# Kernel optimization log

Measured on AMD Instinct MI355X. Metric: run time of the kernel, lower is better.

Reference implementation:

```python
import jax, jax.numpy as jnp
import numpy as np

B_SZ = 8
D_MODEL = 512
D_STATE = 64
N2 = D_STATE // 2  # S4D uses complex-conjugate pairs -> d_state//2 complex modes
L_SEQ = 2048


def setup_inputs() -> dict:
    key = jax.random.key(0)
    ks = jax.random.split(key, 16)
    d = D_MODEL
    scale = 1.0 / np.sqrt(d)
    inp = {
        "x": jax.random.normal(ks[0], (B_SZ, d, L_SEQ), dtype=jnp.float32),
        # q/k/v projections (nn.Linear: weight (out,in), bias (out,))
        "Wq": jax.random.normal(ks[1], (d, d), dtype=jnp.float32) * scale,
        "bq": jax.random.normal(ks[2], (d,), dtype=jnp.float32) * scale,
        "Wk": jax.random.normal(ks[3], (d, d), dtype=jnp.float32) * scale,
        "bk": jax.random.normal(ks[4], (d,), dtype=jnp.float32) * scale,
        "Wv": jax.random.normal(ks[5], (d, d), dtype=jnp.float32) * scale,
        "bv": jax.random.normal(ks[6], (d,), dtype=jnp.float32) * scale,
        # Shift layer params
        "shift_C": jax.random.normal(ks[7], (1, d, D_STATE), dtype=jnp.float32),
        "shift_D": jax.random.normal(ks[8], (d,), dtype=jnp.float32),
        # S4D (diagonal SSM) params
        "log_dt": jax.random.uniform(ks[9], (d,), dtype=jnp.float32,
                                      minval=np.log(1e-3), maxval=np.log(1e-1)),
        "A_real": jnp.log(0.5 * jnp.ones((d, N2), dtype=jnp.float32)),
        "A_imag": jnp.broadcast_to(np.pi * jnp.arange(N2, dtype=jnp.float32), (d, N2)),
        "C_re": jax.random.normal(ks[10], (d, N2), dtype=jnp.float32) * np.sqrt(0.5),
        "C_im": jax.random.normal(ks[11], (d, N2), dtype=jnp.float32) * np.sqrt(0.5),
        "s4_D": jax.random.normal(ks[12], (d,), dtype=jnp.float32),
    }
    return inp


def _linear_chan(x, W, b):
    # x: (B, H, L); Linear applied over channel dim H -> (B, H_out, L)
    return jnp.einsum("bhl,dh->bdl", x, W) + b[:, None]


def _shift(u, C, Dp):
    """Shift SSM: causal conv with kernel = first L taps of C (computed via FFT
    exactly as the torch source does). u: (B, H, L)."""
    L = u.shape[-1]
    n = 2 * L
    H, S = C.shape[1], C.shape[2]
    Bmat = jnp.zeros((H, S), dtype=u.dtype).at[:, 0].set(1.0)
    B_fc = jnp.conj(jnp.fft.rfft(Bmat, n=n, axis=-1))  # (H, L+1)
    C_f = jnp.fft.rfft(C, n=n, axis=-1)                # (1, H, L+1)
    kernel = jnp.fft.irfft(B_fc * C_f, n=n, axis=-1)[..., :L]  # (1, H, L)
    kernel_f = jnp.fft.rfft(kernel, n=n, axis=-1)      # (1, H, L+1)
    u_f = jnp.fft.rfft(u, n=n, axis=-1)                # (B, H, L+1)
    y = jnp.fft.irfft(u_f * kernel_f, n=n, axis=-1)[..., :L]
    return y + u * Dp[:, None]


def _s4d(u, log_dt, A_real, A_imag, C_re, C_im, Dp):
    """Standard S4D forward: ZOH-discretized diagonal SSM kernel + FFT conv.
    u: (B, H, L)."""
    L = u.shape[-1]
    n = 2 * L
    dt = jnp.exp(log_dt)[:, None]                  # (H, 1)
    A = -jnp.exp(A_real) + 1j * A_imag             # (H, N2)
    dtA = A * dt                                   # (H, N2)
    C = (C_re + 1j * C_im) * (jnp.exp(dtA) - 1.0) / A
    vand = jnp.exp(dtA[:, :, None] * jnp.arange(L))  # (H, N2, L)
    K = 2.0 * jnp.einsum("hn,hnl->hl", C, vand).real  # (H, L)
    y = jnp.fft.irfft(jnp.fft.rfft(u, n=n, axis=-1) * jnp.fft.rfft(K, n=n, axis=-1),
                      n=n, axis=-1)[..., :L]
    return y + u * Dp[:, None]


def reference(x, Wq, bq, Wk, bk, Wv, bv, shift_C, shift_D,
              log_dt, A_real, A_imag, C_re, C_im, s4_D):
    q = _linear_chan(x, Wq, bq)
    k = _linear_chan(x, Wk, bk)
    v = _linear_chan(x, Wv, bv)
    shift_out = _shift(k, shift_C, shift_D)
    s4d_out = _s4d(v * shift_out, log_dt, A_real, A_imag, C_re, C_im, s4_D)
    return q * s4d_out
```

## Files before the change

kernel.cpp:

```cpp
#include <hip/hip_runtime.h>
#include <cstdint>


#define DMODEL 512
#define LSEQ 2048

typedef _Float16 half_t;
typedef __attribute__((ext_vector_type(4))) _Float16 half4v;
typedef __attribute__((ext_vector_type(8))) _Float16 half8v;
typedef __attribute__((ext_vector_type(4))) float floatx4;

#define SW(R, c) ((R) * 64 + ((((c) >> 3) ^ ((R) & 7)) << 3) + ((c) & 7))

__device__ __forceinline__ void gload_lds16(const half_t* g, half_t* l) {
  __builtin_amdgcn_global_load_lds(
      (const __attribute__((address_space(1))) uint32_t*)g,
      (__attribute__((address_space(3))) uint32_t*)l, 16, 0, 0);
}

__global__ __launch_bounds__(256) void convert_w(
    const float* __restrict__ Wq, const float* __restrict__ Wk,
    const float* __restrict__ Wv, half_t* __restrict__ W16) {
  int i = blockIdx.x * 256 + threadIdx.x;
  const float* src = (i < 262144) ? Wq : ((i < 524288) ? Wk : Wv);
  int j = i & 262143;
  W16[i] = (half_t)src[j];
}

__global__ __launch_bounds__(256) void transpose_x(
    const float* __restrict__ x, half_t* __restrict__ xT) {
  __shared__ float tile[64][68];
  int b = blockIdx.z;
  int d0 = blockIdx.y * 64;
  int l0 = blockIdx.x * 64;
  int t = threadIdx.x;
  int dy = t >> 4, lx = t & 15;
  const float* xp = x + ((size_t)(b * 512 + d0)) * 2048 + l0;
#pragma unroll
  for (int rr = 0; rr < 4; rr++) {
    float4 v = *(const float4*)(xp + (size_t)(rr * 16 + dy) * 2048 + lx * 4);
    *(float4*)&tile[rr * 16 + dy][lx * 4] = v;
  }
  __syncthreads();
  half_t* op = xT + ((size_t)(b * 2048 + l0)) * 512 + d0;
  int lr = t >> 2, c4 = t & 3;
#pragma unroll
  for (int cc = 0; cc < 2; cc++) {
    int ch = cc * 4 + c4;
    half8v hv;
#pragma unroll
    for (int e = 0; e < 8; e++) hv[e] = (half_t)tile[ch * 8 + e][lr];
    *(half8v*)(op + (size_t)lr * 512 + ch * 8) = hv;
  }
}

__global__ __launch_bounds__(256) void s4d_tables(
    const float* __restrict__ log_dt, const float* __restrict__ A_real,
    const float* __restrict__ A_imag, const float* __restrict__ C_re,
    const float* __restrict__ C_im, const float* __restrict__ shC,
    half_t* __restrict__ Vt, half_t* __restrict__ Et, half_t* __restrict__ Tt,
    half_t* __restrict__ T1t, half_t* __restrict__ T2t,
    float* __restrict__ wt2) {
  __shared__ float aL[32], bL[32], wrL[32], wiL[32], crL[32], ciL[32];
  __shared__ float Kt[64], tapl[64];
  int h = blockIdx.x;
  int tid = threadIdx.x;
  if (tid < 64) { Kt[tid] = 0.f; tapl[tid] = shC[h * 64 + tid]; }
  if (tid < 32) {
    int n = tid, hn = h * 32 + n;
    float dt = expf(log_dt[h]);
    float Ar = -expf(A_real[hn]), Ai = A_imag[hn];
    float a = dt * Ar, b = dt * Ai;
    float ea = expf(a);
    float wr = ea * cosf(b), wi = ea * sinf(b);
    float Am2 = Ar * Ar + Ai * Ai;
    float zr = wr - 1.0f, zi = wi;
    float qr = (zr * Ar + zi * Ai) / Am2;
    float qi = (zi * Ar - zr * Ai) / Am2;
    aL[n] = a; bL[n] = b; wrL[n] = wr; wiL[n] = wi;
    crL[n] = C_re[hn] * qr - C_im[hn] * qi;
    ciL[n] = C_re[hn] * qi + C_im[hn] * qr;
    float e64 = expf(64.0f * a);
    wt2[h * 64 + 2 * n]     = e64 * cosf(64.0f * b);
    wt2[h * 64 + 2 * n + 1] = e64 * sinf(64.0f * b);
  }
  __syncthreads();
  size_t base = (size_t)h * 4096;
  {
    int r = tid >> 2;
    int nb = (tid & 3) * 8;
    float ksum = 0.f;
#pragma unroll
    for (int i = 0; i < 8; i++) {
      int n = nb + i;
      float a = aL[n], b = bL[n];
      float cr = crL[n], ci = ciL[n];
      float er = expf(a * (float)r);
      float w0r = er * cosf(b * (float)r), w0i = er * sinf(b * (float)r);
      ksum += 2.f * (cr * w0r - ci * w0i);
      float wr = wrL[n], wi = wiL[n];
      float w1r = w0r * wr - w0i * wi, w1i = w0r * wi + w0i * wr;
      Et[base + SW(r, 2 * n)]     = (half_t)(2.f * (cr * w1r - ci * w1i));
      Et[base + SW(r, 2 * n + 1)] = (half_t)(-2.f * (cr * w1i + ci * w1r));
      Vt[base + SW(2 * n, 63 - r)]     = (half_t)w0r;
      Vt[base + SW(2 * n + 1, 63 - r)] = (half_t)w0i;
    }
    atomicAdd(&Kt[r], ksum);
  }
  __syncthreads();
#pragma unroll
  for (int e = 0; e < 16; e++) {
    int idx = e * 256 + tid;
    int r = idx >> 6, t = idx & 63;
    int d = r - t;
    size_t a = base + SW(r, t);
    Tt[a]  = (d >= 0) ? (half_t)Kt[d] : (half_t)0.f;
    T1t[a] = (d >= 0) ? (half_t)tapl[d] : (half_t)0.f;
    T2t[a] = (d < 0) ? (half_t)tapl[64 + d] : (half_t)0.f;
  }
}

__global__ __launch_bounds__(256) void gemm_qkv(
    const half_t* __restrict__ xT, const half_t* __restrict__ Wstk,
    const float* __restrict__ bq, const float* __restrict__ bk,
    const float* __restrict__ bv, half_t* __restrict__ outq,
    half_t* __restrict__ outk, half_t* __restrict__ outv) {
  __shared__ half_t smem[16384];
  half_t* As = smem;
  half_t* Bs = smem + 8192;
  int flat = blockIdx.x;
  int swz = (flat & 7) * 192 + (flat >> 3);
  int nt = swz / 12, mt = swz - nt * 12;
  int n0 = nt * 128, m0 = mt * 128;
  int tid = threadIdx.x;
  int lane = tid & 63, wid = tid >> 6;
  int wr = wid >> 1, wc = wid & 1;
  int lrow = lane & 15, lg = lane >> 4;
  int rsub = lane >> 3, ssub = lane & 7;
  int gslot = ssub ^ rsub;

  floatx4 acc[4][4];
#pragma unroll
  for (int i = 0; i < 4; i++)
#pragma unroll
    for (int j = 0; j < 4; j++) acc[i][j] = (floatx4){0.f, 0.f, 0.f, 0.f};

  const half_t* gA = Wstk + (size_t)(m0 + wid * 32 + rsub) * 512 + gslot * 8;
  const half_t* gB = xT + (size_t)(n0 + wid * 32 + rsub) * 512 + gslot * 8;

  for (int kk = 0; kk < 512; kk += 64) {
#pragma unroll
    for (int i = 0; i < 4; i++) {
      int c = wid * 4 + i;
      gload_lds16(gA + (size_t)i * 8 * 512 + kk, As + c * 512);
      gload_lds16(gB + (size_t)i * 8 * 512 + kk, Bs + c * 512);
    }
    __syncthreads();
#pragma unroll
    for (int h = 0; h < 2; h++) {
      half8v af[4], bf[4];
#pragma unroll
      for (int i = 0; i < 4; i++) {
        int r = wr * 64 + i * 16 + lrow;
        af[i] = *(const half8v*)(As + r * 64 + ((h * 4 + lg) ^ (r & 7)) * 8);
      }
#pragma unroll
      for (int j = 0; j < 4; j++) {
        int r = wc * 64 + j * 16 + lrow;
        bf[j] = *(const half8v*)(Bs + r * 64 + ((h * 4 + lg) ^ (r & 7)) * 8);
      }
#pragma unroll
      for (int i = 0; i < 4; i++)
#pragma unroll
        for (int j = 0; j < 4; j++)
          acc[i][j] = __builtin_amdgcn_mfma_f32_16x16x32_f16(af[i], bf[j],
                                                             acc[i][j], 0, 0, 0);
    }
    __syncthreads();
  }

  int z = m0 >> 9;
  const float* bias = (z == 0) ? bq : ((z == 1) ? bk : bv);
  half_t* smemC = smem;
#pragma unroll
  for (int i = 0; i < 4; i++) {
    int dl = wr * 64 + i * 16 + 4 * lg;
    float4 b4 = *(const float4*)&bias[(m0 + dl) & 511];
#pragma unroll
    for (int j = 0; j < 4; j++) {
      int ll = wc * 64 + j * 16 + lrow;
#pragma unroll
      for (int reg = 0; reg < 4; reg++) {
        int d = dl + reg;
        float val = acc[i][j][reg] + ((const float*)&b4)[reg];
        smemC[d * 128 + (((ll >> 3) ^ (d & 15)) << 3) + (ll & 7)] = (half_t)val;
      }
    }
  }
  __syncthreads();
  {
    int t4 = tid >> 4, ch = tid & 15;
    int b = n0 >> 11, l0 = n0 & 2047;
    half_t* outp = (z == 0) ? outq : ((z == 1) ? outk : outv);
#pragma unroll
    for (int rep = 0; rep < 8; rep++) {
      int d = rep * 16 + t4;
      half8v v = *(const half8v*)(smemC + d * 128 + ((ch ^ (d & 15)) << 3));
      size_t rowb = ((size_t)(b * 512 + ((m0 + d) & 511))) * 2048;
      if (z == 0) {
        *(half8v*)(outp + rowb + l0 + ch * 8) = v;
      } else {
        int j = (l0 >> 6) + (ch >> 3);
        int s = ch & 7;
        *(half8v*)(outp + rowb + j * 64 + ((s ^ (j & 7)) << 3)) = v;
      }
    }
  }
}

__global__ __launch_bounds__(256) void s4d_main(
    const half_t* __restrict__ kimg, const half_t* __restrict__ vimg,
    const half_t* __restrict__ T1t, const half_t* __restrict__ T2t,
    const half_t* __restrict__ Vt, const half_t* __restrict__ Et,
    const half_t* __restrict__ Tt, const float* __restrict__ wt2,
    const float* __restrict__ shD, const float* __restrict__ s4D,
    const half_t* __restrict__ qbuf, float* __restrict__ outp) {
  __shared__ half_t kl[33 * 64];
  __shared__ half_t vg[32 * 64];
  __shared__ half_t uh[32 * 64];
  __shared__ half_t tab0[64 * 64];
  __shared__ half_t tab1[64 * 64];
  __shared__ half_t tab2[64 * 64];
  __shared__ float SG[32 * 66];
  int bh = blockIdx.x;
  int h = bh & 511;
  int tid = threadIdx.x;
  int lane = tid & 63, wid = tid >> 6;
  int lrow = lane & 15, lg = lane >> 4;
  int mi = wid & 1;
  int ri0 = wid >> 1;

  {
    const half_t* kp = kimg + (size_t)bh * 2048;
    const half_t* vp = vimg + (size_t)bh * 2048;
    size_t tb = (size_t)h * 4096;
    gload_lds16(kp + wid * 512 + lane * 8, kl + 64 + wid * 512);
    gload_lds16(vp + wid * 512 + lane * 8, vg + wid * 512);
#pragma unroll
    for (int i = 0; i < 2; i++) {
      int c = wid * 2 + i;
      gload_lds16(T1t + tb + c * 512 + lane * 8, tab0 + c * 512);
      gload_lds16(T2t + tb + c * 512 + lane * 8, tab1 + c * 512);
      gload_lds16(Vt + tb + c * 512 + lane * 8, tab2 + c * 512);
    }
  }
  if (tid < 8) {
    half8v zz = {(_Float16)0, (_Float16)0, (_Float16)0, (_Float16)0,
                 (_Float16)0, (_Float16)0, (_Float16)0, (_Float16)0};
    *(half8v*)(kl + tid * 8) = zz;
  }
  float sDsh = shD[h];
  float sD4 = s4D[h];
  __syncthreads();

#define LDF(base, r, ks, key) \
  (*(const half8v*)((base) + (r) * 64 + (((ks) * 4 + lg) ^ (key)) * 8))

  floatx4 acc[2];
  acc[0] = (floatx4){0.f, 0.f, 0.f, 0.f};
  acc[1] = (floatx4){0.f, 0.f, 0.f, 0.f};
  {
    int jA = mi * 16 + lrow;
    int key1 = lrow & 7, key2 = (lrow + 7) & 7;
#pragma unroll
    for (int ks = 0; ks < 2; ks++) {
      half8v a1 = LDF(kl, 1 + jA, ks, key1);
      half8v a2 = LDF(kl, jA, ks, key2);
#pragma unroll
      for (int tt = 0; tt < 2; tt++) {
        int rb = (ri0 + tt * 2) * 16 + lrow;
        half8v b1 = LDF(tab0, rb, ks, lrow & 7);
        half8v b2 = LDF(tab1, rb, ks, lrow & 7);
        acc[tt] = __builtin_amdgcn_mfma_f32_16x16x32_f16(a1, b1, acc[tt], 0, 0, 0);
        acc[tt] = __builtin_amdgcn_mfma_f32_16x16x32_f16(a2, b2, acc[tt], 0, 0, 0);
      }
    }
  }
#pragma unroll
  for (int tt = 0; tt < 2; tt++) {
#pragma unroll
    for (int reg = 0; reg < 4; reg++) {
      int j = mi * 16 + 4 * lg + reg;
      int r = (ri0 + tt * 2) * 16 + lrow;
      int cph = (((r >> 3) ^ (j & 7)) << 3) + (r & 7);
      float kvv = (float)kl[(1 + j) * 64 + cph];
      float vvv = (float)vg[j * 64 + cph];
      uh[j * 64 + cph] = (half_t)(vvv * (acc[tt][reg] + sDsh * kvv));
    }
  }
  __syncthreads();

  {
    size_t tb = (size_t)h * 4096;
#pragma unroll
    for (int i = 0; i < 2; i++) {
      int c = wid * 2 + i;
      gload_lds16(Et + tb + c * 512 + lane * 8, tab0 + c * 512);
      gload_lds16(Tt + tb + c * 512 + lane * 8, tab1 + c * 512);
    }
  }

  acc[0] = (floatx4){0.f, 0.f, 0.f, 0.f};
  acc[1] = (floatx4){0.f, 0.f, 0.f, 0.f};
#pragma unroll
  for (int ks = 0; ks < 2; ks++) {
    half8v a = LDF(uh, mi * 16 + lrow, ks, lrow & 7);
#pragma unroll
    for (int tt = 0; tt < 2; tt++) {
      int rb = (ri0 + tt * 2) * 16 + lrow;
      half8v b = LDF(tab2, rb, ks, lrow & 7);
      acc[tt] = __builtin_amdgcn_mfma_f32_16x16x32_f16(a, b, acc[tt], 0, 0, 0);
    }
  }
#pragma unroll
  for (int tt = 0; tt < 2; tt++) {
    int ri = ri0 + tt * 2;
#pragma unroll
    for (int reg = 0; reg < 4; reg++) {
      int j = mi * 16 + 4 * lg + reg;
      SG[j * 66 + ri * 16 + lrow] = acc[tt][reg];
    }
  }
  __syncthreads();

  if (tid < 32) {
    int n = tid;
    float wTr = wt2[h * 64 + 2 * n], wTi = wt2[h * 64 + 2 * n + 1];
    float gr = 0.f, gi = 0.f;
    for (int j = 0; j < 32; j++) {
      float tr = SG[j * 66 + 2 * n], ti = SG[j * 66 + 2 * n + 1];
      SG[j * 66 + 2 * n] = gr; SG[j * 66 + 2 * n + 1] = gi;
      float nr = wTr * gr - wTi * gi + tr;
      gi = wTr * gi + wTi * gr + ti;
      gr = nr;
    }
  }
  __syncthreads();

  {
    int j = tid >> 3, s = tid & 7;
    half8v g;
#pragma unroll
    for (int i = 0; i < 8; i++) g[i] = (half_t)SG[j * 66 + s * 8 + i];
    *(half8v*)(vg + j * 64 + (s ^ (j & 7)) * 8) = g;
  }
  __syncthreads();

  acc[0] = (floatx4){0.f, 0.f, 0.f, 0.f};
  acc[1] = (floatx4){0.f, 0.f, 0.f, 0.f};
#pragma unroll
  for (int ks = 0; ks < 2; ks++) {
    half8v ag = LDF(vg, mi * 16 + lrow, ks, lrow & 7);
    half8v au = LDF(uh, mi * 16 + lrow, ks, lrow & 7);
#pragma unroll
    for (int tt = 0; tt < 2; tt++) {
      int rb = (ri0 + tt * 2) * 16 + lrow;
      half8v be = LDF(tab0, rb, ks, lrow & 7);
      half8v bt = LDF(tab1, rb, ks, lrow & 7);
      acc[tt] = __builtin_amdgcn_mfma_f32_16x16x32_f16(ag, be, acc[tt], 0, 0, 0);
      acc[tt] = __builtin_amdgcn_mfma_f32_16x16x32_f16(au, bt, acc[tt], 0, 0, 0);
    }
  }
#pragma unroll
  for (int tt = 0; tt < 2; tt++) {
#pragma unroll
    for (int reg = 0; reg < 4; reg++) {
      int j = mi * 16 + 4 * lg + reg;
      int r = (ri0 + tt * 2) * 16 + lrow;
      int cph = (((r >> 3) ^ (j & 7)) << 3) + (r & 7);
      SG[j * 64 + r] = acc[tt][reg] + sD4 * (float)uh[j * 64 + cph];
    }
  }
  __syncthreads();

  {
    const half_t* qp = qbuf + (size_t)bh * 2048;
    float* op = outp + (size_t)bh * 2048;
    half8v qv = *(const half8v*)(qp + tid * 8);
    float4 o0, o1;
    o0.x = (float)qv[0] * SG[tid * 8 + 0];
    o0.y = (float)qv[1] * SG[tid * 8 + 1];
    o0.z = (float)qv[2] * SG[tid * 8 + 2];
    o0.w = (float)qv[3] * SG[tid * 8 + 3];
    o1.x = (float)qv[4] * SG[tid * 8 + 4];
    o1.y = (float)qv[5] * SG[tid * 8 + 5];
    o1.z = (float)qv[6] * SG[tid * 8 + 6];
    o1.w = (float)qv[7] * SG[tid * 8 + 7];
    *(float4*)(op + tid * 8) = o0;
    *(float4*)(op + tid * 8 + 4) = o1;
  }
#undef LDF
}

extern "C" void kernel_launch(void* const* d_in, const int* in_sizes, int n_in,
                              void* d_out, int out_size, void* d_ws, size_t ws_size,
                              hipStream_t stream) {
  const float* x      = (const float*)d_in[0];
  const float* Wq     = (const float*)d_in[1];
  const float* bq     = (const float*)d_in[2];
  const float* Wk     = (const float*)d_in[3];
  const float* bk     = (const float*)d_in[4];
  const float* Wv     = (const float*)d_in[5];
  const float* bv     = (const float*)d_in[6];
  const float* shC    = (const float*)d_in[7];
  const float* shD    = (const float*)d_in[8];
  const float* log_dt = (const float*)d_in[9];
  const float* A_real = (const float*)d_in[10];
  const float* A_imag = (const float*)d_in[11];
  const float* C_re   = (const float*)d_in[12];
  const float* C_im   = (const float*)d_in[13];
  const float* s4D    = (const float*)d_in[14];
  float* out = (float*)d_out;
  half_t* wsh = (half_t*)d_ws;

  half_t* qbuf = wsh;
  half_t* kbuf = wsh + 8388608;
  half_t* vbuf = wsh + 16777216;
  half_t* xT16 = wsh + 25165824;
  half_t* W16  = wsh + 33554432;
  half_t* Vt   = wsh + 34340864;
  half_t* Et   = wsh + 36438016;
  half_t* Tt   = wsh + 38535168;
  half_t* T1t  = wsh + 40632320;
  half_t* T2t  = wsh + 42729472;
  float*  wt2  = (float*)(wsh + 44826624);

  convert_w<<<3072, 256, 0, stream>>>(Wq, Wk, Wv, W16);
  transpose_x<<<dim3(32, 8, 8), 256, 0, stream>>>(x, xT16);
  s4d_tables<<<512, 256, 0, stream>>>(log_dt, A_real, A_imag, C_re, C_im, shC,
                                      Vt, Et, Tt, T1t, T2t, wt2);
  gemm_qkv<<<dim3(1536), 256, 0, stream>>>(xT16, W16, bq, bk, bv,
                                           qbuf, kbuf, vbuf);
  s4d_main<<<4096, 256, 0, stream>>>(kbuf, vbuf, T1t, T2t, Vt, Et, Tt,
                                     wt2, shD, s4D, qbuf, out);
}
```

Before: 95.85 us.

## Triple-buffer QKV GEMM with larger 256x128 tiles and direct epilogue stores

The QKV GEMM moves to 512-thread blocks computing 256x128 tiles. The K loop now runs a three-stage LDS ring (144KB dynamic shared memory) that prefetches two k-steps ahead, interleaves global-to-LDS loads with MFMA, and raises wave priority around the MFMA blocks, so the per-step barrier stalls are hidden. The LDS-staged epilogue is replaced by direct per-element scalar half stores from the accumulators. Those narrow, scattered stores risk poor write coalescing, and the large LDS footprint limits occupancy to one block per CU.

```diff
diff --git a/kernel.cpp b/kernel.cpp
--- a/kernel.cpp
+++ b/kernel.cpp
@@ -120,24 +120,25 @@
   }
 }
 
-__global__ __launch_bounds__(256) void gemm_qkv(
+__global__ __launch_bounds__(512) void gemm_qkv(
     const half_t* __restrict__ xT, const half_t* __restrict__ Wstk,
     const float* __restrict__ bq, const float* __restrict__ bk,
     const float* __restrict__ bv, half_t* __restrict__ outq,
     half_t* __restrict__ outk, half_t* __restrict__ outv) {
-  __shared__ half_t smem[16384];
-  half_t* As = smem;
-  half_t* Bs = smem + 8192;
+  extern __shared__ half_t smem[];
   int flat = blockIdx.x;
-  int swz = (flat & 7) * 192 + (flat >> 3);
-  int nt = swz / 12, mt = swz - nt * 12;
-  int n0 = nt * 128, m0 = mt * 128;
+  int swz = (flat & 7) * 96 + (flat >> 3);
+  int mt = swz % 6, nt = swz / 6;
+  int m0 = mt * 256, n0 = nt * 128;
   int tid = threadIdx.x;
   int lane = tid & 63, wid = tid >> 6;
-  int wr = wid >> 1, wc = wid & 1;
+  int wm = wid & 3, wn = wid >> 2;
   int lrow = lane & 15, lg = lane >> 4;
-  int rsub = lane >> 3, ssub = lane & 7;
-  int gslot = ssub ^ rsub;
+  int rS = tid >> 3;
+  int sS = (tid & 7) ^ (rS & 7);
+
+  const half_t* gA = Wstk + (size_t)(m0 + rS) * 512 + sS * 8;
+  const half_t* gB = xT + (size_t)(n0 + rS) * 512 + sS * 8;
 
   floatx4 acc[4][4];
 #pragma unroll
@@ -145,74 +146,102 @@
 #pragma unroll
     for (int j = 0; j < 4; j++) acc[i][j] = (floatx4){0.f, 0.f, 0.f, 0.f};
 
-  const half_t* gA = Wstk + (size_t)(m0 + wid * 32 + rsub) * 512 + gslot * 8;
-  const half_t* gB = xT + (size_t)(n0 + wid * 32 + rsub) * 512 + gslot * 8;
-
-  for (int kk = 0; kk < 512; kk += 64) {
-#pragma unroll
-    for (int i = 0; i < 4; i++) {
-      int c = wid * 4 + i;
-      gload_lds16(gA + (size_t)i * 8 * 512 + kk, As + c * 512);
-      gload_lds16(gB + (size_t)i * 8 * 512 + kk, Bs + c * 512);
-    }
-    __syncthreads();
-#pragma unroll
-    for (int h = 0; h < 2; h++) {
-      half8v af[4], bf[4];
-#pragma unroll
-      for (int i = 0; i < 4; i++) {
-        int r = wr * 64 + i * 16 + lrow;
-        af[i] = *(const half8v*)(As + r * 64 + ((h * 4 + lg) ^ (r & 7)) * 8);
-      }
-#pragma unroll
-      for (int j = 0; j < 4; j++) {
-        int r = wc * 64 + j * 16 + lrow;
-        bf[j] = *(const half8v*)(Bs + r * 64 + ((h * 4 + lg) ^ (r & 7)) * 8);
-      }
-#pragma unroll
-      for (int i = 0; i < 4; i++)
-#pragma unroll
-        for (int j = 0; j < 4; j++)
-          acc[i][j] = __builtin_amdgcn_mfma_f32_16x16x32_f16(af[i], bf[j],
-                                                             acc[i][j], 0, 0, 0);
-    }
-    __syncthreads();
-  }
+#define STAGE_A(b, kt, ld)                                                    \
+  gload_lds16(gA + (size_t)(ld) * 64 * 512 + (kt) * 64,                       \
+              smem + (b) * 24576 + ((ld) * 512 + tid) * 8)
+#define STAGE_B(b, kt, ld)                                                    \
+  gload_lds16(gB + (size_t)(ld) * 64 * 512 + (kt) * 64,                       \
+              smem + (b) * 24576 + 16384 + ((ld) * 512 + tid) * 8)
+
+  STAGE_A(0, 0, 0); STAGE_A(0, 0, 1); STAGE_A(0, 0, 2); STAGE_A(0, 0, 3);
+  STAGE_B(0, 0, 0); STAGE_B(0, 0, 1);
+  STAGE_A(1, 1, 0); STAGE_A(1, 1, 1); STAGE_A(1, 1, 2); STAGE_A(1, 1, 3);
+  STAGE_B(1, 1, 0); STAGE_B(1, 1, 1);
+  asm volatile("s_waitcnt vmcnt(6)" ::: "memory");
+  __builtin_amdgcn_s_barrier();
+  __builtin_amdgcn_sched_barrier(0);
+
+  int cur = 0;
+  for (int t = 0; t < 8; t++) {
+    const half_t* Ab = smem + cur * 24576;
+    const half_t* Bb = Ab + 16384;
+    int wb = cur + 2; if (wb >= 3) wb -= 3;
+
+    half8v bf[4][2], af[2][2];
+#pragma unroll
+    for (int nj = 0; nj < 4; nj++) {
+      int rb = wn * 64 + nj * 16 + lrow;
+#pragma unroll
+      for (int ks = 0; ks < 2; ks++)
+        bf[nj][ks] = *(const half8v*)(Bb + rb * 64 + (((ks * 4 + lg) ^ (rb & 7)) << 3));
+    }
+#pragma unroll
+    for (int i = 0; i < 2; i++) {
+      int ra = wm * 64 + i * 16 + lrow;
+#pragma unroll
+      for (int ks = 0; ks < 2; ks++)
+        af[i][ks] = *(const half8v*)(Ab + ra * 64 + (((ks * 4 + lg) ^ (ra & 7)) << 3));
+    }
+    if (t < 6) { STAGE_A(wb, t + 2, 0); STAGE_A(wb, t + 2, 1); STAGE_A(wb, t + 2, 2); }
+    __builtin_amdgcn_s_setprio(1);
+#pragma unroll
+    for (int i = 0; i < 2; i++)
+#pragma unroll
+      for (int nj = 0; nj < 4; nj++)
+#pragma unroll
+        for (int ks = 0; ks < 2; ks++)
+          acc[i][nj] = __builtin_amdgcn_mfma_f32_16x16x32_f16(af[i][ks], bf[nj][ks],
+                                                              acc[i][nj], 0, 0, 0);
+    __builtin_amdgcn_s_setprio(0);
+
+#pragma unroll
+    for (int i = 0; i < 2; i++) {
+      int ra = wm * 64 + (2 + i) * 16 + lrow;
+#pragma unroll
+      for (int ks = 0; ks < 2; ks++)
+        af[i][ks] = *(const half8v*)(Ab + ra * 64 + (((ks * 4 + lg) ^ (ra & 7)) << 3));
+    }
+    if (t < 6) { STAGE_A(wb, t + 2, 3); STAGE_B(wb, t + 2, 0); STAGE_B(wb, t + 2, 1); }
+    __builtin_amdgcn_s_setprio(1);
+#pragma unroll
+    for (int i = 0; i < 2; i++)
+#pragma unroll
+      for (int nj = 0; nj < 4; nj++)
+#pragma unroll
+        for (int ks = 0; ks < 2; ks++)
+          acc[2 + i][nj] = __builtin_amdgcn_mfma_f32_16x16x32_f16(af[i][ks], bf[nj][ks],
+                                                                  acc[2 + i][nj], 0, 0, 0);
+    __builtin_amdgcn_s_setprio(0);
+
+    if (t < 6)       asm volatile("s_waitcnt vmcnt(6)" ::: "memory");
+    else if (t == 6) asm volatile("s_waitcnt vmcnt(0)" ::: "memory");
+    __builtin_amdgcn_s_barrier();
+    __builtin_amdgcn_sched_barrier(0);
+    cur = cur + 1; if (cur >= 3) cur -= 3;
+  }
+#undef STAGE_A
+#undef STAGE_B
 
   int z = m0 >> 9;
   const float* bias = (z == 0) ? bq : ((z == 1) ? bk : bv);
-  half_t* smemC = smem;
-#pragma unroll
-  for (int i = 0; i < 4; i++) {
-    int dl = wr * 64 + i * 16 + 4 * lg;
-    float4 b4 = *(const float4*)&bias[(m0 + dl) & 511];
-#pragma unroll
-    for (int j = 0; j < 4; j++) {
-      int ll = wc * 64 + j * 16 + lrow;
+  half_t* outp = (z == 0) ? outq : ((z == 1) ? outk : outv);
+#pragma unroll
+  for (int mi = 0; mi < 4; mi++) {
+    int d = (m0 + wm * 64 + mi * 16 + 4 * lg) & 511;
+#pragma unroll
+    for (int nj = 0; nj < 4; nj++) {
+      int n = n0 + wn * 64 + nj * 16 + lrow;
+      int b = n >> 11, l = n & 2047;
 #pragma unroll
       for (int reg = 0; reg < 4; reg++) {
-        int d = dl + reg;
-        float val = acc[i][j][reg] + ((const float*)&b4)[reg];
-        smemC[d * 128 + (((ll >> 3) ^ (d & 15)) << 3) + (ll & 7)] = (half_t)val;
-      }
-    }
-  }
-  __syncthreads();
-  {
-    int t4 = tid >> 4, ch = tid & 15;
-    int b = n0 >> 11, l0 = n0 & 2047;
-    half_t* outp = (z == 0) ? outq : ((z == 1) ? outk : outv);
-#pragma unroll
-    for (int rep = 0; rep < 8; rep++) {
-      int d = rep * 16 + t4;
-      half8v v = *(const half8v*)(smemC + d * 128 + ((ch ^ (d & 15)) << 3));
-      size_t rowb = ((size_t)(b * 512 + ((m0 + d) & 511))) * 2048;
-      if (z == 0) {
-        *(half8v*)(outp + rowb + l0 + ch * 8) = v;
-      } else {
-        int j = (l0 >> 6) + (ch >> 3);
-        int s = ch & 7;
-        *(half8v*)(outp + rowb + j * 64 + ((s ^ (j & 7)) << 3)) = v;
+        float val = acc[mi][nj][reg] + bias[d + reg];
+        size_t bhbase = ((size_t)(b * 512 + d + reg)) * 2048;
+        if (z == 0) {
+          outp[bhbase + l] = (half_t)val;
+        } else {
+          int jj = l >> 6, c = l & 63;
+          outp[bhbase + SW(jj, c)] = (half_t)val;
+        }
       }
     }
   }
@@ -435,12 +464,15 @@
   half_t* T2t  = wsh + 42729472;
   float*  wt2  = (float*)(wsh + 44826624);
 
+  hipFuncSetAttribute((const void*)gemm_qkv,
+                      hipFuncAttributeMaxDynamicSharedMemorySize, 147456);
+
   convert_w<<<3072, 256, 0, stream>>>(Wq, Wk, Wv, W16);
   transpose_x<<<dim3(32, 8, 8), 256, 0, stream>>>(x, xT16);
   s4d_tables<<<512, 256, 0, stream>>>(log_dt, A_real, A_imag, C_re, C_im, shC,
                                       Vt, Et, Tt, T1t, T2t, wt2);
-  gemm_qkv<<<dim3(1536), 256, 0, stream>>>(xT16, W16, bq, bk, bv,
-                                           qbuf, kbuf, vbuf);
+  gemm_qkv<<<dim3(768), 512, 147456, stream>>>(xT16, W16, bq, bk, bv,
+                                               qbuf, kbuf, vbuf);
   s4d_main<<<4096, 256, 0, stream>>>(kbuf, vbuf, T1t, T2t, Vt, Et, Tt,
                                      wt2, shD, s4D, qbuf, out);
 }
```

Result: slower. 99.29 us (+3.6%).

## Merge prep kernels and make s4d_main loop over batches with double-buffered loads

Applied to the files above, without the earlier changes.

The three prep kernels (weight conversion, x transpose, S4D table build) become one launch whose work is split by block-index range. s4d_main now runs one block per channel and loops over all 8 batches. It loads the five per-channel tables into LDS once and double-buffers the next batch's k/v tiles with async global-to-LDS loads. This cuts launch overhead and redundant table reloads, but leaves only 512 blocks, which lowers parallelism and latency hiding on a large GPU.

```diff
diff --git a/kernel.cpp b/kernel.cpp
--- a/kernel.cpp
+++ b/kernel.cpp
@@ -18,105 +18,114 @@
       (__attribute__((address_space(3))) uint32_t*)l, 16, 0, 0);
 }
 
-__global__ __launch_bounds__(256) void convert_w(
-    const float* __restrict__ Wq, const float* __restrict__ Wk,
-    const float* __restrict__ Wv, half_t* __restrict__ W16) {
-  int i = blockIdx.x * 256 + threadIdx.x;
-  const float* src = (i < 262144) ? Wq : ((i < 524288) ? Wk : Wv);
-  int j = i & 262143;
-  W16[i] = (half_t)src[j];
-}
-
-__global__ __launch_bounds__(256) void transpose_x(
-    const float* __restrict__ x, half_t* __restrict__ xT) {
-  __shared__ float tile[64][68];
-  int b = blockIdx.z;
-  int d0 = blockIdx.y * 64;
-  int l0 = blockIdx.x * 64;
-  int t = threadIdx.x;
-  int dy = t >> 4, lx = t & 15;
-  const float* xp = x + ((size_t)(b * 512 + d0)) * 2048 + l0;
-#pragma unroll
-  for (int rr = 0; rr < 4; rr++) {
-    float4 v = *(const float4*)(xp + (size_t)(rr * 16 + dy) * 2048 + lx * 4);
-    *(float4*)&tile[rr * 16 + dy][lx * 4] = v;
-  }
-  __syncthreads();
-  half_t* op = xT + ((size_t)(b * 2048 + l0)) * 512 + d0;
-  int lr = t >> 2, c4 = t & 3;
-#pragma unroll
-  for (int cc = 0; cc < 2; cc++) {
-    int ch = cc * 4 + c4;
-    half8v hv;
-#pragma unroll
-    for (int e = 0; e < 8; e++) hv[e] = (half_t)tile[ch * 8 + e][lr];
-    *(half8v*)(op + (size_t)lr * 512 + ch * 8) = hv;
-  }
-}
-
-__global__ __launch_bounds__(256) void s4d_tables(
+#define WAIT_LGKM_BAR()                                   \
+  do {                                                    \
+    asm volatile("s_waitcnt lgkmcnt(0)" ::: "memory");    \
+    __builtin_amdgcn_s_barrier();                         \
+    __builtin_amdgcn_sched_barrier(0);                    \
+  } while (0)
+
+__global__ __launch_bounds__(256) void prep(
+    const float* __restrict__ x, const float* __restrict__ Wq,
+    const float* __restrict__ Wk, const float* __restrict__ Wv,
     const float* __restrict__ log_dt, const float* __restrict__ A_real,
     const float* __restrict__ A_imag, const float* __restrict__ C_re,
     const float* __restrict__ C_im, const float* __restrict__ shC,
+    half_t* __restrict__ xT, half_t* __restrict__ W16,
     half_t* __restrict__ Vt, half_t* __restrict__ Et, half_t* __restrict__ Tt,
     half_t* __restrict__ T1t, half_t* __restrict__ T2t,
     float* __restrict__ wt2) {
+  __shared__ float tile[64][68];
   __shared__ float aL[32], bL[32], wrL[32], wiL[32], crL[32], ciL[32];
   __shared__ float Kt[64], tapl[64];
-  int h = blockIdx.x;
+  int bid = blockIdx.x;
   int tid = threadIdx.x;
-  if (tid < 64) { Kt[tid] = 0.f; tapl[tid] = shC[h * 64 + tid]; }
-  if (tid < 32) {
-    int n = tid, hn = h * 32 + n;
-    float dt = expf(log_dt[h]);
-    float Ar = -expf(A_real[hn]), Ai = A_imag[hn];
-    float a = dt * Ar, b = dt * Ai;
-    float ea = expf(a);
-    float wr = ea * cosf(b), wi = ea * sinf(b);
-    float Am2 = Ar * Ar + Ai * Ai;
-    float zr = wr - 1.0f, zi = wi;
-    float qr = (zr * Ar + zi * Ai) / Am2;
-    float qi = (zi * Ar - zr * Ai) / Am2;
-    aL[n] = a; bL[n] = b; wrL[n] = wr; wiL[n] = wi;
-    crL[n] = C_re[hn] * qr - C_im[hn] * qi;
-    ciL[n] = C_re[hn] * qi + C_im[hn] * qr;
-    float e64 = expf(64.0f * a);
-    wt2[h * 64 + 2 * n]     = e64 * cosf(64.0f * b);
-    wt2[h * 64 + 2 * n + 1] = e64 * sinf(64.0f * b);
-  }
-  __syncthreads();
-  size_t base = (size_t)h * 4096;
-  {
-    int r = tid >> 2;
-    int nb = (tid & 3) * 8;
-    float ksum = 0.f;
-#pragma unroll
-    for (int i = 0; i < 8; i++) {
-      int n = nb + i;
-      float a = aL[n], b = bL[n];
-      float cr = crL[n], ci = ciL[n];
-      float er = expf(a * (float)r);
-      float w0r = er * cosf(b * (float)r), w0i = er * sinf(b * (float)r);
-      ksum += 2.f * (cr * w0r - ci * w0i);
-      float wr = wrL[n], wi = wiL[n];
-      float w1r = w0r * wr - w0i * wi, w1i = w0r * wi + w0i * wr;
-      Et[base + SW(r, 2 * n)]     = (half_t)(2.f * (cr * w1r - ci * w1i));
-      Et[base + SW(r, 2 * n + 1)] = (half_t)(-2.f * (cr * w1i + ci * w1r));
-      Vt[base + SW(2 * n, 63 - r)]     = (half_t)w0r;
-      Vt[base + SW(2 * n + 1, 63 - r)] = (half_t)w0i;
-    }
-    atomicAdd(&Kt[r], ksum);
-  }
-  __syncthreads();
-#pragma unroll
-  for (int e = 0; e < 16; e++) {
-    int idx = e * 256 + tid;
-    int r = idx >> 6, t = idx & 63;
-    int d = r - t;
-    size_t a = base + SW(r, t);
-    Tt[a]  = (d >= 0) ? (half_t)Kt[d] : (half_t)0.f;
-    T1t[a] = (d >= 0) ? (half_t)tapl[d] : (half_t)0.f;
-    T2t[a] = (d < 0) ? (half_t)tapl[64 + d] : (half_t)0.f;
+
+  if (bid < 512) {
+    int h = bid;
+    if (tid < 64) { Kt[tid] = 0.f; tapl[tid] = shC[h * 64 + tid]; }
+    if (tid < 32) {
+      int n = tid, hn = h * 32 + n;
+      float dt = expf(log_dt[h]);
+      float Ar = -expf(A_real[hn]), Ai = A_imag[hn];
+      float a = dt * Ar, b = dt * Ai;
+      float ea = expf(a);
+      float wr = ea * cosf(b), wi = ea * sinf(b);
+      float Am2 = Ar * Ar + Ai * Ai;
+      float zr = wr - 1.0f, zi = wi;
+      float qr = (zr * Ar + zi * Ai) / Am2;
+      float qi = (zi * Ar - zr * Ai) / Am2;
+      aL[n] = a; bL[n] = b; wrL[n] = wr; wiL[n] = wi;
+      crL[n] = C_re[hn] * qr - C_im[hn] * qi;
+      ciL[n] = C_re[hn] * qi + C_im[hn] * qr;
+      float e64 = expf(64.0f * a);
+      wt2[h * 64 + 2 * n]     = e64 * cosf(64.0f * b);
+      wt2[h * 64 + 2 * n + 1] = e64 * sinf(64.0f * b);
+    }
+    __syncthreads();
+    size_t base = (size_t)h * 4096;
+    {
+      int r = tid >> 2;
+      int nb = (tid & 3) * 8;
+      float ksum = 0.f;
+#pragma unroll
+      for (int i = 0; i < 8; i++) {
+        int n = nb + i;
+        float a = aL[n], b = bL[n];
+        float cr = crL[n], ci = ciL[n];
+        float er = expf(a * (float)r);
+        float w0r = er * cosf(b * (float)r), w0i = er * sinf(b * (float)r);
+        ksum += 2.f * (cr * w0r - ci * w0i);
+        float wr = wrL[n], wi = wiL[n];
+        float w1r = w0r * wr - w0i * wi, w1i = w0r * wi + w0i * wr;
+        Et[base + SW(r, 2 * n)]     = (half_t)(2.f * (cr * w1r - ci * w1i));
+        Et[base + SW(r, 2 * n + 1)] = (half_t)(-2.f * (cr * w1i + ci * w1r));
+        Vt[base + SW(2 * n, 63 - r)]     = (half_t)w0r;
+        Vt[base + SW(2 * n + 1, 63 - r)] = (half_t)w0i;
+      }
+      atomicAdd(&Kt[r], ksum);
+    }
+    __syncthreads();
+#pragma unroll
+    for (int e = 0; e < 16; e++) {
+      int idx = e * 256 + tid;
+      int r = idx >> 6, t = idx & 63;
+      int d = r - t;
+      size_t a = base + SW(r, t);
+      Tt[a]  = (d >= 0) ? (half_t)Kt[d] : (half_t)0.f;
+      T1t[a] = (d >= 0) ? (half_t)tapl[d] : (half_t)0.f;
+      T2t[a] = (d < 0) ? (half_t)tapl[64 + d] : (half_t)0.f;
+    }
+  } else if (bid < 2560) {
+    int i = bid - 512;
+    int b = i >> 8, rem = i & 255;
+    int d0 = (rem >> 5) * 64, l0 = (rem & 31) * 64;
+    int dy = tid >> 4, lx = tid & 15;
+    const float* xp = x + ((size_t)(b * 512 + d0)) * 2048 + l0;
+#pragma unroll
+    for (int rr = 0; rr < 4; rr++) {
+      float4 v = *(const float4*)(xp + (size_t)(rr * 16 + dy) * 2048 + lx * 4);
+      *(float4*)&tile[rr * 16 + dy][lx * 4] = v;
+    }
+    __syncthreads();
+    half_t* op = xT + ((size_t)(b * 2048 + l0)) * 512 + d0;
+    int lr = tid >> 2, c4 = tid & 3;
+#pragma unroll
+    for (int cc = 0; cc < 2; cc++) {
+      int ch = cc * 4 + c4;
+      half8v hv;
+#pragma unroll
+      for (int e = 0; e < 8; e++) hv[e] = (half_t)tile[ch * 8 + e][lr];
+      *(half8v*)(op + (size_t)lr * 512 + ch * 8) = hv;
+    }
+  } else {
+    int base = (bid - 2560) * 256 + tid;
+#pragma unroll
+    for (int it = 0; it < 6; it++) {
+      int i = base + it * 131072;
+      const float* src = (i < 262144) ? Wq : ((i < 524288) ? Wk : Wv);
+      W16[i] = (half_t)src[i & 262143];
+    }
   }
 }
 
@@ -225,179 +234,191 @@
     const half_t* __restrict__ Tt, const float* __restrict__ wt2,
     const float* __restrict__ shD, const float* __restrict__ s4D,
     const half_t* __restrict__ qbuf, float* __restrict__ outp) {
-  __shared__ half_t kl[33 * 64];
-  __shared__ half_t vg[32 * 64];
+  __shared__ half_t tabs[5][4096];
+  __shared__ half_t kl[2][33 * 64];
+  __shared__ half_t vg[2][32 * 64];
   __shared__ half_t uh[32 * 64];
-  __shared__ half_t tab0[64 * 64];
-  __shared__ half_t tab1[64 * 64];
-  __shared__ half_t tab2[64 * 64];
   __shared__ float SG[32 * 66];
-  int bh = blockIdx.x;
-  int h = bh & 511;
+  int h = blockIdx.x;
   int tid = threadIdx.x;
   int lane = tid & 63, wid = tid >> 6;
   int lrow = lane & 15, lg = lane >> 4;
-  int mi = wid & 1;
-  int ri0 = wid >> 1;
+  int mi = wid & 1, ri0 = wid >> 1;
 
   {
-    const half_t* kp = kimg + (size_t)bh * 2048;
-    const half_t* vp = vimg + (size_t)bh * 2048;
     size_t tb = (size_t)h * 4096;
-    gload_lds16(kp + wid * 512 + lane * 8, kl + 64 + wid * 512);
-    gload_lds16(vp + wid * 512 + lane * 8, vg + wid * 512);
 #pragma unroll
     for (int i = 0; i < 2; i++) {
       int c = wid * 2 + i;
-      gload_lds16(T1t + tb + c * 512 + lane * 8, tab0 + c * 512);
-      gload_lds16(T2t + tb + c * 512 + lane * 8, tab1 + c * 512);
-      gload_lds16(Vt + tb + c * 512 + lane * 8, tab2 + c * 512);
-    }
-  }
-  if (tid < 8) {
+      gload_lds16(T1t + tb + c * 512 + lane * 8, &tabs[0][c * 512]);
+      gload_lds16(T2t + tb + c * 512 + lane * 8, &tabs[1][c * 512]);
+      gload_lds16(Vt  + tb + c * 512 + lane * 8, &tabs[2][c * 512]);
+      gload_lds16(Et  + tb + c * 512 + lane * 8, &tabs[3][c * 512]);
+      gload_lds16(Tt  + tb + c * 512 + lane * 8, &tabs[4][c * 512]);
+    }
+    gload_lds16(kimg + (size_t)h * 2048 + wid * 512 + lane * 8,
+                &kl[0][64 + wid * 512]);
+    gload_lds16(vimg + (size_t)h * 2048 + wid * 512 + lane * 8,
+                &vg[0][wid * 512]);
+  }
+  if (tid < 16) {
     half8v zz = {(_Float16)0, (_Float16)0, (_Float16)0, (_Float16)0,
                  (_Float16)0, (_Float16)0, (_Float16)0, (_Float16)0};
-    *(half8v*)(kl + tid * 8) = zz;
+    *(half8v*)(&kl[tid >> 3][(tid & 7) * 8]) = zz;
   }
   float sDsh = shD[h];
   float sD4 = s4D[h];
-  __syncthreads();
+  float wTr = wt2[h * 64 + 2 * (tid & 31)];
+  float wTi = wt2[h * 64 + 2 * (tid & 31) + 1];
+  const half_t* t1 = tabs[0];
+  const half_t* t2 = tabs[1];
+  const half_t* tV = tabs[2];
+  const half_t* tE = tabs[3];
+  const half_t* tT = tabs[4];
 
 #define LDF(base, r, ks, key) \
   (*(const half8v*)((base) + (r) * 64 + (((ks) * 4 + lg) ^ (key)) * 8))
 
-  floatx4 acc[2];
-  acc[0] = (floatx4){0.f, 0.f, 0.f, 0.f};
-  acc[1] = (floatx4){0.f, 0.f, 0.f, 0.f};
-  {
-    int jA = mi * 16 + lrow;
-    int key1 = lrow & 7, key2 = (lrow + 7) & 7;
+  int cur = 0;
+  for (int bi = 0; bi < 8; bi++) {
+    if (bi < 7) {
+      size_t nb = (size_t)((bi + 1) * 512 + h) * 2048;
+      gload_lds16(kimg + nb + wid * 512 + lane * 8, &kl[cur ^ 1][64 + wid * 512]);
+      gload_lds16(vimg + nb + wid * 512 + lane * 8, &vg[cur ^ 1][wid * 512]);
+      asm volatile("s_waitcnt vmcnt(2) lgkmcnt(0)" ::: "memory");
+    } else {
+      asm volatile("s_waitcnt vmcnt(0) lgkmcnt(0)" ::: "memory");
+    }
+    __builtin_amdgcn_s_barrier();
+    __builtin_amdgcn_sched_barrier(0);
+
+    const half_t* klc = kl[cur];
+    half_t* vgc = vg[cur];
+    floatx4 acc[2];
+
+    acc[0] = (floatx4){0.f, 0.f, 0.f, 0.f};
+    acc[1] = (floatx4){0.f, 0.f, 0.f, 0.f};
+    {
+      int jA = mi * 16 + lrow;
+      int key1 = lrow & 7, key2 = (lrow + 7) & 7;
+#pragma unroll
+      for (int ks = 0; ks < 2; ks++) {
+        half8v a1 = LDF(klc, 1 + jA, ks, key1);
+        half8v a2 = LDF(klc, jA, ks, key2);
+#pragma unroll
+        for (int tt = 0; tt < 2; tt++) {
+          int rb = (ri0 + tt * 2) * 16 + lrow;
+          half8v b1 = LDF(t1, rb, ks, lrow & 7);
+          half8v b2 = LDF(t2, rb, ks, lrow & 7);
+          acc[tt] = __builtin_amdgcn_mfma_f32_16x16x32_f16(a1, b1, acc[tt], 0, 0, 0);
+          acc[tt] = __builtin_amdgcn_mfma_f32_16x16x32_f16(a2, b2, acc[tt], 0, 0, 0);
+        }
+      }
+    }
+#pragma unroll
+    for (int tt = 0; tt < 2; tt++) {
+#pragma unroll
+      for (int reg = 0; reg < 4; reg++) {
+        int j = mi * 16 + 4 * lg + reg;
+        int r = (ri0 + tt * 2) * 16 + lrow;
+        int cph = (((r >> 3) ^ (j & 7)) << 3) + (r & 7);
+        float kvv = (float)klc[(1 + j) * 64 + cph];
+        float vvv = (float)vgc[j * 64 + cph];
+        uh[j * 64 + cph] = (half_t)(vvv * (acc[tt][reg] + sDsh * kvv));
+      }
+    }
+    WAIT_LGKM_BAR();
+
+    acc[0] = (floatx4){0.f, 0.f, 0.f, 0.f};
+    acc[1] = (floatx4){0.f, 0.f, 0.f, 0.f};
 #pragma unroll
     for (int ks = 0; ks < 2; ks++) {
-      half8v a1 = LDF(kl, 1 + jA, ks, key1);
-      half8v a2 = LDF(kl, jA, ks, key2);
+      half8v a = LDF(uh, mi * 16 + lrow, ks, lrow & 7);
 #pragma unroll
       for (int tt = 0; tt < 2; tt++) {
         int rb = (ri0 + tt * 2) * 16 + lrow;
-        half8v b1 = LDF(tab0, rb, ks, lrow & 7);
-        half8v b2 = LDF(tab1, rb, ks, lrow & 7);
-        acc[tt] = __builtin_amdgcn_mfma_f32_16x16x32_f16(a1, b1, acc[tt], 0, 0, 0);
-        acc[tt] = __builtin_amdgcn_mfma_f32_16x16x32_f16(a2, b2, acc[tt], 0, 0, 0);
-      }
-    }
-  }
-#pragma unroll
-  for (int tt = 0; tt < 2; tt++) {
-#pragma unroll
-    for (int reg = 0; reg < 4; reg++) {
-      int j = mi * 16 + 4 * lg + reg;
-      int r = (ri0 + tt * 2) * 16 + lrow;
-      int cph = (((r >> 3) ^ (j & 7)) << 3) + (r & 7);
-      float kvv = (float)kl[(1 + j) * 64 + cph];
-      float vvv = (float)vg[j * 64 + cph];
-      uh[j * 64 + cph] = (half_t)(vvv * (acc[tt][reg] + sDsh * kvv));
-    }
-  }
-  __syncthreads();
-
-  {
-    size_t tb = (size_t)h * 4096;
-#pragma unroll
-    for (int i = 0; i < 2; i++) {
-      int c = wid * 2 + i;
-      gload_lds16(Et + tb + c * 512 + lane * 8, tab0 + c * 512);
-      gload_lds16(Tt + tb + c * 512 + lane * 8, tab1 + c * 512);
-    }
-  }
-
-  acc[0] = (floatx4){0.f, 0.f, 0.f, 0.f};
-  acc[1] = (floatx4){0.f, 0.f, 0.f, 0.f};
-#pragma unroll
-  for (int ks = 0; ks < 2; ks++) {
-    half8v a = LDF(uh, mi * 16 + lrow, ks, lrow & 7);
+        half8v b = LDF(tV, rb, ks, lrow & 7);
+        acc[tt] = __builtin_amdgcn_mfma_f32_16x16x32_f16(a, b, acc[tt], 0, 0, 0);
+      }
+    }
 #pragma unroll
     for (int tt = 0; tt < 2; tt++) {
-      int rb = (ri0 + tt * 2) * 16 + lrow;
-      half8v b = LDF(tab2, rb, ks, lrow & 7);
-      acc[tt] = __builtin_amdgcn_mfma_f32_16x16x32_f16(a, b, acc[tt], 0, 0, 0);
-    }
-  }
-#pragma unroll
-  for (int tt = 0; tt < 2; tt++) {
-    int ri = ri0 + tt * 2;
-#pragma unroll
-    for (int reg = 0; reg < 4; reg++) {
-      int j = mi * 16 + 4 * lg + reg;
-      SG[j * 66 + ri * 16 + lrow] = acc[tt][reg];
-    }
-  }
-  __syncthreads();
-
-  if (tid < 32) {
-    int n = tid;
-    float wTr = wt2[h * 64 + 2 * n], wTi = wt2[h * 64 + 2 * n + 1];
-    float gr = 0.f, gi = 0.f;
-    for (int j = 0; j < 32; j++) {
-      float tr = SG[j * 66 + 2 * n], ti = SG[j * 66 + 2 * n + 1];
-      SG[j * 66 + 2 * n] = gr; SG[j * 66 + 2 * n + 1] = gi;
-      float nr = wTr * gr - wTi * gi + tr;
-      gi = wTr * gi + wTi * gr + ti;
-      gr = nr;
-    }
-  }
-  __syncthreads();
-
-  {
-    int j = tid >> 3, s = tid & 7;
-    half8v g;
-#pragma unroll
-    for (int i = 0; i < 8; i++) g[i] = (half_t)SG[j * 66 + s * 8 + i];
-    *(half8v*)(vg + j * 64 + (s ^ (j & 7)) * 8) = g;
-  }
-  __syncthreads();
-
-  acc[0] = (floatx4){0.f, 0.f, 0.f, 0.f};
-  acc[1] = (floatx4){0.f, 0.f, 0.f, 0.f};
-#pragma unroll
-  for (int ks = 0; ks < 2; ks++) {
-    half8v ag = LDF(vg, mi * 16 + lrow, ks, lrow & 7);
-    half8v au = LDF(uh, mi * 16 + lrow, ks, lrow & 7);
+      int ri = ri0 + tt * 2;
+#pragma unroll
+      for (int reg = 0; reg < 4; reg++) {
+        int j = mi * 16 + 4 * lg + reg;
+        SG[j * 66 + ri * 16 + lrow] = acc[tt][reg];
+      }
+    }
+    WAIT_LGKM_BAR();
+
+    if (tid < 32) {
+      int n = tid;
+      float gr = 0.f, gi = 0.f;
+      for (int j = 0; j < 32; j++) {
+        float tr = SG[j * 66 + 2 * n], ti = SG[j * 66 + 2 * n + 1];
+        SG[j * 66 + 2 * n] = gr; SG[j * 66 + 2 * n + 1] = gi;
+        float nr = wTr * gr - wTi * gi + tr;
+        gi = wTr * gi + wTi * gr + ti;
+        gr = nr;
+      }
+    }
+    WAIT_LGKM_BAR();
+
+    {
+      int j = tid >> 3, s = tid & 7;
+      half8v g;
+#pragma unroll
+      for (int i = 0; i < 8; i++) g[i] = (half_t)SG[j * 66 + s * 8 + i];
+      *(half8v*)(vgc + j * 64 + (s ^ (j & 7)) * 8) = g;
+    }
+    WAIT_LGKM_BAR();
+
+    acc[0] = (floatx4){0.f, 0.f, 0.f, 0.f};
+    acc[1] = (floatx4){0.f, 0.f, 0.f, 0.f};
+#pragma unroll
+    for (int ks = 0; ks < 2; ks++) {
+      half8v ag = LDF(vgc, mi * 16 + lrow, ks, lrow & 7);
+      half8v au = LDF(uh, mi * 16 + lrow, ks, lrow & 7);
+#pragma unroll
+      for (int tt = 0; tt < 2; tt++) {
+        int rb = (ri0 + tt * 2) * 16 + lrow;
+        half8v be = LDF(tE, rb, ks, lrow & 7);
+        half8v bt = LDF(tT, rb, ks, lrow & 7);
+        acc[tt] = __builtin_amdgcn_mfma_f32_16x16x32_f16(ag, be, acc[tt], 0, 0, 0);
+        acc[tt] = __builtin_amdgcn_mfma_f32_16x16x32_f16(au, bt, acc[tt], 0, 0, 0);
+      }
+    }
 #pragma unroll
     for (int tt = 0; tt < 2; tt++) {
-      int rb = (ri0 + tt * 2) * 16 + lrow;
-      half8v be = LDF(tab0, rb, ks, lrow & 7);
-      half8v bt = LDF(tab1, rb, ks, lrow & 7);
-      acc[tt] = __builtin_amdgcn_mfma_f32_16x16x32_f16(ag, be, acc[tt], 0, 0, 0);
-      acc[tt] = __builtin_amdgcn_mfma_f32_16x16x32_f16(au, bt, acc[tt], 0, 0, 0);
-    }
-  }
-#pragma unroll
-  for (int tt = 0; tt < 2; tt++) {
-#pragma unroll
-    for (int reg = 0; reg < 4; reg++) {
-      int j = mi * 16 + 4 * lg + reg;
-      int r = (ri0 + tt * 2) * 16 + lrow;
-      int cph = (((r >> 3) ^ (j & 7)) << 3) + (r & 7);
-      SG[j * 64 + r] = acc[tt][reg] + sD4 * (float)uh[j * 64 + cph];
-    }
-  }
-  __syncthreads();
-
-  {
-    const half_t* qp = qbuf + (size_t)bh * 2048;
-    float* op = outp + (size_t)bh * 2048;
-    half8v qv = *(const half8v*)(qp + tid * 8);
-    float4 o0, o1;
-    o0.x = (float)qv[0] * SG[tid * 8 + 0];
-    o0.y = (float)qv[1] * SG[tid * 8 + 1];
-    o0.z = (float)qv[2] * SG[tid * 8 + 2];
-    o0.w = (float)qv[3] * SG[tid * 8 + 3];
-    o1.x = (float)qv[4] * SG[tid * 8 + 4];
-    o1.y = (float)qv[5] * SG[tid * 8 + 5];
-    o1.z = (float)qv[6] * SG[tid * 8 + 6];
-    o1.w = (float)qv[7] * SG[tid * 8 + 7];
-    *(float4*)(op + tid * 8) = o0;
-    *(float4*)(op + tid * 8 + 4) = o1;
+#pragma unroll
+      for (int reg = 0; reg < 4; reg++) {
+        int j = mi * 16 + 4 * lg + reg;
+        int r = (ri0 + tt * 2) * 16 + lrow;
+        int cph = (((r >> 3) ^ (j & 7)) << 3) + (r & 7);
+        SG[j * 64 + r] = acc[tt][reg] + sD4 * (float)uh[j * 64 + cph];
+      }
+    }
+    WAIT_LGKM_BAR();
+
+    {
+      size_t bh = (size_t)(bi * 512 + h) * 2048;
+      half8v qv = *(const half8v*)(qbuf + bh + tid * 8);
+      float* op = outp + bh;
+      float4 o0, o1;
+      o0.x = (float)qv[0] * SG[tid * 8 + 0];
+      o0.y = (float)qv[1] * SG[tid * 8 + 1];
+      o0.z = (float)qv[2] * SG[tid * 8 + 2];
+      o0.w = (float)qv[3] * SG[tid * 8 + 3];
+      o1.x = (float)qv[4] * SG[tid * 8 + 4];
+      o1.y = (float)qv[5] * SG[tid * 8 + 5];
+      o1.z = (float)qv[6] * SG[tid * 8 + 6];
+      o1.w = (float)qv[7] * SG[tid * 8 + 7];
+      *(float4*)(op + tid * 8) = o0;
+      *(float4*)(op + tid * 8 + 4) = o1;
+    }
+    WAIT_LGKM_BAR();
+    cur ^= 1;
   }
 #undef LDF
 }
@@ -435,12 +456,11 @@
   half_t* T2t  = wsh + 42729472;
   float*  wt2  = (float*)(wsh + 44826624);
 
-  convert_w<<<3072, 256, 0, stream>>>(Wq, Wk, Wv, W16);
-  transpose_x<<<dim3(32, 8, 8), 256, 0, stream>>>(x, xT16);
-  s4d_tables<<<512, 256, 0, stream>>>(log_dt, A_real, A_imag, C_re, C_im, shC,
-                                      Vt, Et, Tt, T1t, T2t, wt2);
+  prep<<<3072, 256, 0, stream>>>(x, Wq, Wk, Wv, log_dt, A_real, A_imag,
+                                 C_re, C_im, shC, xT16, W16,
+                                 Vt, Et, Tt, T1t, T2t, wt2);
   gemm_qkv<<<dim3(1536), 256, 0, stream>>>(xT16, W16, bq, bk, bv,
                                            qbuf, kbuf, vbuf);
-  s4d_main<<<4096, 256, 0, stream>>>(kbuf, vbuf, T1t, T2t, Vt, Et, Tt,
-                                     wt2, shD, s4D, qbuf, out);
+  s4d_main<<<512, 256, 0, stream>>>(kbuf, vbuf, T1t, T2t, Vt, Et, Tt,
+                                    wt2, shD, s4D, qbuf, out);
 }
```

After: 86.13 us. 10.1% less time.
